# Performance work log

Measured on AMD Instinct MI355X. Metric: run time of the kernel, lower is better.

## Reference

```python
import jax, jax.numpy as jnp
import numpy as np

H = 16        # num_attention_heads
D = 1024      # hidden_size
HD = D // H   # head_dim = 64


def setup_inputs() -> dict:
    key = jax.random.key(0)
    ks = jax.random.split(key, 5)
    B, T = 16, 1024
    s_in = 1.0 / np.sqrt(D)
    return {
        "hidden_states": jax.random.normal(ks[0], (B, T, D), dtype=jnp.float32),
        "w_qkv": jax.random.normal(ks[1], (D, 3 * D), dtype=jnp.float32) * s_in,
        "b_qkv": jnp.zeros((3 * D,), dtype=jnp.float32),
        "w_out": jax.random.normal(ks[2], (D, D), dtype=jnp.float32) * s_in,
        "b_out": jnp.zeros((D,), dtype=jnp.float32),
    }


def reference(hidden_states, w_qkv, b_qkv, w_out, b_out):
    B, T, C = hidden_states.shape
    qkv = hidden_states @ w_qkv + b_qkv                      # [B,T,3C]
    q, k, v = jnp.split(qkv, 3, axis=-1)
    # [B,T,C] -> [B,H,T,HD]
    q = q.reshape(B, T, H, HD).transpose(0, 2, 1, 3)
    k = k.reshape(B, T, H, HD).transpose(0, 2, 1, 3)
    v = v.reshape(B, T, H, HD).transpose(0, 2, 1, 3)
    scale = 1.0 / np.sqrt(HD)
    logits = jnp.einsum("bhqd,bhkd->bhqk", q, k) * scale     # [B,H,T,T]
    attn = jax.nn.softmax(logits, axis=-1)
    out = jnp.einsum("bhqk,bhkd->bhqd", attn, v)             # [B,H,T,HD]
    out = out.transpose(0, 2, 1, 3).reshape(B, T, C)
    return out @ w_out + b_out
```

## Files before the change

kernel.cpp:

```cpp
#include <hip/hip_runtime.h>
#include <cstdint>
#include <cstddef>

typedef _Float16 h8 __attribute__((ext_vector_type(8)));
typedef _Float16 h4 __attribute__((ext_vector_type(4)));
typedef float f4 __attribute__((ext_vector_type(4)));
typedef float fx16 __attribute__((ext_vector_type(16)));

#define MFMA(a, b, c) __builtin_amdgcn_mfma_f32_16x16x32_f16((a), (b), (c), 0, 0, 0)
#define MFMA32(a, b, c) __builtin_amdgcn_mfma_f32_32x32x16_f16((a), (b), (c), 0, 0, 0)

__device__ __forceinline__ void gl_lds16(const void* g, void* l) {
  __builtin_amdgcn_global_load_lds((const __attribute__((address_space(1))) void*)g,
                                   (__attribute__((address_space(3))) void*)l, 16, 0, 0);
}

__global__ void k_cvt_hs(const float* __restrict__ in, _Float16* __restrict__ out, int n8) {
  int i = blockIdx.x * blockDim.x + threadIdx.x;
  if (i >= n8) return;
  size_t idx = (size_t)i * 8;
  float4 a = *(const float4*)(in + idx);
  float4 b = *(const float4*)(in + idx + 4);
  h8 o;
  o[0] = (_Float16)a.x; o[1] = (_Float16)a.y; o[2] = (_Float16)a.z; o[3] = (_Float16)a.w;
  o[4] = (_Float16)b.x; o[5] = (_Float16)b.y; o[6] = (_Float16)b.z; o[7] = (_Float16)b.w;
  *(h8*)(out + idx) = o;
}

__global__ void k_transcvt(const float* __restrict__ in, _Float16* __restrict__ out, int N, int K) {
  __shared__ float tile[64 * 65];
  int tn = blockIdx.x * 64, tk = blockIdx.y * 64;
  for (int i = 0; i < 4; ++i) {
    int cid = i * 256 + threadIdx.x;
    int r = cid >> 4, c4 = cid & 15;
    float4 v = *(const float4*)(in + (size_t)(tk + r) * N + tn + c4 * 4);
    tile[r * 65 + c4 * 4 + 0] = v.x; tile[r * 65 + c4 * 4 + 1] = v.y;
    tile[r * 65 + c4 * 4 + 2] = v.z; tile[r * 65 + c4 * 4 + 3] = v.w;
  }
  __syncthreads();
  for (int i = 0; i < 2; ++i) {
    int cid = i * 256 + threadIdx.x;
    int n = cid >> 3, kc = cid & 7;
    h8 o;
    for (int j = 0; j < 8; ++j) o[j] = (_Float16)tile[(kc * 8 + j) * 65 + n];
    *(h8*)(out + (size_t)(tn + n) * K + tk + kc * 8) = o;
  }
}

__global__ __launch_bounds__(256) void k_gemm_qkv(
    const _Float16* __restrict__ A, const _Float16* __restrict__ BT,
    const float* __restrict__ bias,
    _Float16* __restrict__ Q, _Float16* __restrict__ Kq, _Float16* __restrict__ Vt) {
  __shared__ char smem[32768];
  _Float16* sA = (_Float16*)smem;
  _Float16* sB = (_Float16*)(smem + 16384);
  const int K = 1024;
  int tid = threadIdx.x, wave = tid >> 6, lane = tid & 63;
  int l31 = lane & 31, l32h = lane >> 5;
  int tm = blockIdx.y * 128, tn = blockIdx.x * 128;
  int wm = (wave & 1) * 64, wn = (wave >> 1) * 64;
  fx16 acc[2][2] = {};
  for (int kt = 0; kt < K; kt += 64) {
    __syncthreads();
    for (int i = 0; i < 4; ++i) {
      int cid = i * 256 + tid;
      int r = cid >> 3, cs = cid & 7, cg = cs ^ (r & 7);
      gl_lds16(A + (size_t)(tm + r) * K + kt + cg * 8, (char*)sA + cid * 16);
      gl_lds16(BT + (size_t)(tn + r) * K + kt + cg * 8, (char*)sB + cid * 16);
    }
    __syncthreads();
    for (int k0 = 0; k0 < 64; k0 += 16) {
      h8 af[2], bf[2];
      int ch = (k0 >> 3) + l32h;
      for (int mi = 0; mi < 2; ++mi) {
        int r = wm + mi * 32 + l31;
        af[mi] = *(const h8*)((const char*)sA + ((r * 8 + (ch ^ (r & 7))) * 16));
      }
      for (int ni = 0; ni < 2; ++ni) {
        int r = wn + ni * 32 + l31;
        bf[ni] = *(const h8*)((const char*)sB + ((r * 8 + (ch ^ (r & 7))) * 16));
      }
      for (int mi = 0; mi < 2; ++mi)
        for (int ni = 0; ni < 2; ++ni)
          acc[mi][ni] = MFMA32(af[mi], bf[ni], acc[mi][ni]);
    }
  }
  if (blockIdx.x < 16) {
    for (int ni = 0; ni < 2; ++ni) {
      int n = tn + wn + ni * 32 + l31;
      float bv = bias[n];
      int which = n >> 10, h = (n >> 6) & 15, d = n & 63;
      _Float16* dst = which == 0 ? Q : Kq;
      for (int mi = 0; mi < 2; ++mi) {
        for (int g = 0; g < 4; ++g) {
          for (int rr = 0; rr < 4; ++rr) {
            int m = tm + wm + mi * 32 + rr + 8 * g + 4 * l32h;
            int b = m >> 10, t = m & 1023;
            dst[(((size_t)b * 16 + h) * 1024 + t) * 64 + d] =
                (_Float16)(acc[mi][ni][g * 4 + rr] + bv);
          }
        }
      }
    }
  } else {
    _Float16* L = (_Float16*)smem;
    int b = tm >> 10, tbase = tm & 1023;
    for (int pass = 0; pass < 2; ++pass) {
      __syncthreads();
      if ((wave & 1) == pass) {
        for (int mi = 0; mi < 2; ++mi) {
          for (int ni = 0; ni < 2; ++ni) {
            int n_local = wn + ni * 32 + l31;
            float bv = bias[tn + n_local];
            for (int g = 0; g < 4; ++g) {
              h4 pk;
              for (int rr = 0; rr < 4; ++rr)
                pk[rr] = (_Float16)(acc[mi][ni][g * 4 + rr] + bv);
              *(h4*)(L + n_local * 68 + mi * 32 + 8 * g + 4 * l32h) = pk;
            }
          }
        }
      }
      __syncthreads();
      for (int it = 0; it < 2; ++it) {
        int n_local = it * 64 + (tid >> 2);
        int h = (tn - 2048 + n_local) >> 6;
        int d = n_local & 63;
        size_t row = (((size_t)b * 16 + h) * 64 + d) * 1024 + tbase + pass * 64;
        for (int j = 0; j < 2; ++j) {
          int th = (tid & 3) * 8 + j * 32;
          *(h8*)(Vt + row + th) = *(const h8*)(L + n_local * 68 + th);
        }
      }
    }
  }
}

__global__ __launch_bounds__(256, 2) void k_attn(
    const _Float16* __restrict__ Q, const _Float16* __restrict__ Kk,
    const _Float16* __restrict__ Vt, _Float16* __restrict__ O) {
  __shared__ char smem[32768 + 8192 + 8192];
  _Float16* sQ = (_Float16*)smem;
  _Float16* sP = (_Float16*)smem;
  _Float16* sK = (_Float16*)(smem + 32768);
  _Float16* sV = (_Float16*)(smem + 32768 + 8192);
  const float SCL = 0.125f * 1.44269504088896340736f;
  int tid = threadIdx.x, wave = tid >> 6, lane = tid & 63;
  int l15 = lane & 15, l4 = lane >> 4;
  int bh = blockIdx.y;
  int qt = blockIdx.x * 256;
  const _Float16* Qb = Q + (size_t)bh * 65536;
  const _Float16* Kb = Kk + (size_t)bh * 65536;
  const _Float16* Vb = Vt + (size_t)bh * 65536;

  for (int i = 0; i < 8; ++i) {
    int cid = i * 256 + tid;
    int r = cid >> 3, cs = cid & 7, cg = cs ^ (r & 7);
    gl_lds16(Qb + (size_t)(qt + r) * 64 + cg * 8, (char*)sQ + cid * 16);
  }
  __syncthreads();
  h8 qf[4][2];
  for (int nt = 0; nt < 4; ++nt) {
    int r = wave * 64 + nt * 16 + l15;
    for (int kk = 0; kk < 2; ++kk) {
      int ch = kk * 4 + l4;
      qf[nt][kk] = *(const h8*)((const char*)sQ + ((r * 8 + (ch ^ (r & 7))) * 16));
    }
  }
  _Float16 scl_h = (_Float16)SCL;
  for (int nt = 0; nt < 4; ++nt)
    for (int kk = 0; kk < 2; ++kk)
      for (int j = 0; j < 8; ++j) qf[nt][kk][j] *= scl_h;

  int cid0 = tid, cid1 = tid + 256;
  int r0 = cid0 >> 3, c0 = (cid0 & 7) ^ (r0 & 7);
  int r1 = cid1 >> 3, c1 = (cid1 & 7) ^ (r1 & 7);
  const _Float16* kp0 = Kb + (size_t)r0 * 64 + c0 * 8;
  const _Float16* kp1 = Kb + (size_t)r1 * 64 + c1 * 8;
  const _Float16* vp0 = Vb + (size_t)r0 * 1024 + c0 * 8;
  const _Float16* vp1 = Vb + (size_t)r1 * 1024 + c1 * 8;
  char* dK0 = (char*)sK + cid0 * 16; char* dK1 = (char*)sK + cid1 * 16;
  char* dV0 = (char*)sV + cid0 * 16; char* dV1 = (char*)sV + cid1 * 16;

  f4 oacc[4][4] = {};
  f4 lacc[4] = {};
  h8 ones;
  for (int j = 0; j < 8; ++j) ones[j] = (_Float16)1.0f;
  _Float16* pw = sP + wave * 64 * 40;

  for (int kt = 0; kt < 1024; kt += 64) {
    __syncthreads();
    gl_lds16(kp0, dK0); gl_lds16(kp1, dK1);
    gl_lds16(vp0, dV0); gl_lds16(vp1, dV1);
    kp0 += 4096; kp1 += 4096; vp0 += 64; vp1 += 64;
    __syncthreads();
    for (int mh = 0; mh < 2; ++mh) {
      f4 sacc[2][4] = {};
      for (int kk = 0; kk < 2; ++kk) {
        h8 kf[2];
        int ch = kk * 4 + l4;
        for (int mt = 0; mt < 2; ++mt) {
          int r = mh * 32 + mt * 16 + l15;
          kf[mt] = *(const h8*)((const char*)sK + ((r * 8 + (ch ^ (r & 7))) * 16));
        }
        for (int mt = 0; mt < 2; ++mt)
          for (int nt = 0; nt < 4; ++nt)
            sacc[mt][nt] = MFMA(kf[mt], qf[nt][kk], sacc[mt][nt]);
      }
      for (int mt = 0; mt < 2; ++mt) {
        for (int nt = 0; nt < 4; ++nt) {
          float p0 = exp2f(sacc[mt][nt][0]);
          float p1 = exp2f(sacc[mt][nt][1]);
          float p2 = exp2f(sacc[mt][nt][2]);
          float p3 = exp2f(sacc[mt][nt][3]);
          h4 pk;
          pk[0] = (_Float16)p0; pk[1] = (_Float16)p1;
          pk[2] = (_Float16)p2; pk[3] = (_Float16)p3;
          *(h4*)(pw + (nt * 16 + l15) * 40 + mt * 16 + l4 * 4) = pk;
        }
      }
      h8 pf[4], vf[4];
      for (int mi = 0; mi < 4; ++mi)
        pf[mi] = *(const h8*)(pw + (mi * 16 + l15) * 40 + l4 * 8);
      int ch = mh * 4 + l4;
      for (int nd = 0; nd < 4; ++nd) {
        int r = nd * 16 + l15;
        vf[nd] = *(const h8*)((const char*)sV + ((r * 8 + (ch ^ (r & 7))) * 16));
      }
      for (int mi = 0; mi < 4; ++mi) {
        for (int nd = 0; nd < 4; ++nd)
          oacc[mi][nd] = MFMA(pf[mi], vf[nd], oacc[mi][nd]);
        lacc[mi] = MFMA(pf[mi], ones, lacc[mi]);
      }
    }
  }
  int b = bh >> 4, h = bh & 15;
  for (int mi = 0; mi < 4; ++mi) {
    for (int r = 0; r < 4; ++r) {
      float inv = 1.f / lacc[mi][r];
      int t = qt + wave * 64 + mi * 16 + l4 * 4 + r;
      for (int nd = 0; nd < 4; ++nd)
        O[(size_t)(b * 1024 + t) * 1024 + h * 64 + nd * 16 + l15] =
            (_Float16)(oacc[mi][nd][r] * inv);
    }
  }
}

__global__ __launch_bounds__(256) void k_gemm_out(
    const _Float16* __restrict__ A, const _Float16* __restrict__ BT,
    const float* __restrict__ bias, float* __restrict__ C) {
  __shared__ _Float16 sA[128 * 64];
  __shared__ _Float16 sB[128 * 64];
  const int K = 1024;
  int tid = threadIdx.x, wave = tid >> 6, lane = tid & 63;
  int l31 = lane & 31, l32h = lane >> 5;
  int tm = blockIdx.y * 128, tn = blockIdx.x * 128;
  int wm = (wave & 1) * 64, wn = (wave >> 1) * 64;
  fx16 acc[2][2] = {};
  for (int kt = 0; kt < K; kt += 64) {
    __syncthreads();
    for (int i = 0; i < 4; ++i) {
      int cid = i * 256 + tid;
      int r = cid >> 3, cs = cid & 7, cg = cs ^ (r & 7);
      gl_lds16(A + (size_t)(tm + r) * K + kt + cg * 8, (char*)sA + cid * 16);
      gl_lds16(BT + (size_t)(tn + r) * K + kt + cg * 8, (char*)sB + cid * 16);
    }
    __syncthreads();
    for (int k0 = 0; k0 < 64; k0 += 16) {
      h8 af[2], bf[2];
      int ch = (k0 >> 3) + l32h;
      for (int mi = 0; mi < 2; ++mi) {
        int r = wm + mi * 32 + l31;
        af[mi] = *(const h8*)((const char*)sA + ((r * 8 + (ch ^ (r & 7))) * 16));
      }
      for (int ni = 0; ni < 2; ++ni) {
        int r = wn + ni * 32 + l31;
        bf[ni] = *(const h8*)((const char*)sB + ((r * 8 + (ch ^ (r & 7))) * 16));
      }
      for (int mi = 0; mi < 2; ++mi)
        for (int ni = 0; ni < 2; ++ni)
          acc[mi][ni] = MFMA32(af[mi], bf[ni], acc[mi][ni]);
    }
  }
  for (int ni = 0; ni < 2; ++ni) {
    int n = tn + wn + ni * 32 + l31;
    float bv = bias[n];
    for (int mi = 0; mi < 2; ++mi) {
      for (int g = 0; g < 4; ++g) {
        for (int rr = 0; rr < 4; ++rr) {
          int m = tm + wm + mi * 32 + rr + 8 * g + 4 * l32h;
          C[(size_t)m * 1024 + n] = acc[mi][ni][g * 4 + rr] + bv;
        }
      }
    }
  }
}

extern "C" void kernel_launch(void* const* d_in, const int* in_sizes, int n_in,
                              void* d_out, int out_size, void* d_ws, size_t ws_size,
                              hipStream_t stream) {
  const float* hs    = (const float*)d_in[0];
  const float* w_qkv = (const float*)d_in[1];
  const float* b_qkv = (const float*)d_in[2];
  const float* w_out = (const float*)d_in[3];
  const float* b_out = (const float*)d_in[4];
  float* out = (float*)d_out;
  char* ws = (char*)d_ws;

  _Float16* hs_h  = (_Float16*)(ws);
  _Float16* wqkvT = (_Float16*)(ws + 33554432);
  _Float16* woutT = (_Float16*)(ws + 39845888);
  _Float16* q_ws  = (_Float16*)(ws + 41943040);
  _Float16* k_ws  = (_Float16*)(ws + 75497472);
  _Float16* vt_ws = (_Float16*)(ws + 109051904);

  k_cvt_hs<<<8192, 256, 0, stream>>>(hs, hs_h, 2097152);
  k_transcvt<<<dim3(48, 16), 256, 0, stream>>>(w_qkv, wqkvT, 3072, 1024);
  k_transcvt<<<dim3(16, 16), 256, 0, stream>>>(w_out, woutT, 1024, 1024);
  k_gemm_qkv<<<dim3(24, 128), 256, 0, stream>>>(hs_h, wqkvT, b_qkv, q_ws, k_ws, vt_ws);
  _Float16* attn_h = hs_h;
  k_attn<<<dim3(4, 256), 256, 0, stream>>>(q_ws, k_ws, vt_ws, attn_h);
  k_gemm_out<<<dim3(8, 128), 256, 0, stream>>>(attn_h, woutT, b_out, out);
}
```

Measured before the change: 425.4 us.

## Rewrite projection GEMMs as 256x256 double-buffered pipelined tiles with 512 threads

After: 388.3 us. -8.7%, faster.

```diff
diff --git a/kernel.cpp b/kernel.cpp
--- a/kernel.cpp
+++ b/kernel.cpp
@@ -5,14 +5,22 @@
 typedef _Float16 h8 __attribute__((ext_vector_type(8)));
 typedef _Float16 h4 __attribute__((ext_vector_type(4)));
 typedef float f4 __attribute__((ext_vector_type(4)));
-typedef float fx16 __attribute__((ext_vector_type(16)));
 
 #define MFMA(a, b, c) __builtin_amdgcn_mfma_f32_16x16x32_f16((a), (b), (c), 0, 0, 0)
-#define MFMA32(a, b, c) __builtin_amdgcn_mfma_f32_32x32x16_f16((a), (b), (c), 0, 0, 0)
 
 __device__ __forceinline__ void gl_lds16(const void* g, void* l) {
   __builtin_amdgcn_global_load_lds((const __attribute__((address_space(1))) void*)g,
                                    (__attribute__((address_space(3))) void*)l, 16, 0, 0);
+}
+
+__device__ __forceinline__ h8 lds_frag(const char* base, int r, int ch) {
+  return *(const h8*)(base + ((r * 8 + (ch ^ (r & 7))) * 16));
+}
+
+__device__ __forceinline__ void BAR() {
+  asm volatile("" ::: "memory");
+  __builtin_amdgcn_s_barrier();
+  asm volatile("" ::: "memory");
 }
 
 __global__ void k_cvt_hs(const float* __restrict__ in, _Float16* __restrict__ out, int n8) {
@@ -47,90 +55,184 @@
   }
 }
 
-__global__ __launch_bounds__(256) void k_gemm_qkv(
+__device__ __forceinline__ void gemm256_mainloop(
+    const _Float16* __restrict__ A, const _Float16* __restrict__ BT,
+    char* smem, int tm, int tn, f4 (&acc)[8][4]) {
+  int tid = threadIdx.x, lane = tid & 63, wave = tid >> 6;
+  int l15 = lane & 15, l4 = lane >> 4;
+  int wm = (wave >> 2) * 128, wn = (wave & 3) * 64;
+  const _Float16* Ab = A + (size_t)tm * 1024;
+  const _Float16* Bb = BT + (size_t)tn * 1024;
+  int r0 = tid >> 3, cg = (tid & 7) ^ (r0 & 7);
+  char* cA = smem;           char* nA = smem + 32768;
+  char* cB = smem + 65536;   char* nB = smem + 98304;
+
+  auto stA = [&](int kt, int h, char* dst) {
+    const _Float16* s = Ab + (size_t)(h * 128 + r0) * 1024 + kt + cg * 8;
+    gl_lds16(s, dst + h * 16384 + tid * 16);
+    gl_lds16(s + 64 * 1024, dst + h * 16384 + 8192 + tid * 16);
+  };
+  auto stB = [&](int kt, int h, char* dst) {
+    const _Float16* s = Bb + (size_t)(h * 128 + r0) * 1024 + kt + cg * 8;
+    gl_lds16(s, dst + h * 16384 + tid * 16);
+    gl_lds16(s + 64 * 1024, dst + h * 16384 + 8192 + tid * 16);
+  };
+
+  stA(0, 0, cA); stA(0, 1, cA);
+  stB(0, 0, cB); stB(0, 1, cB);
+  stB(64, 0, nB); stB(64, 1, nB);
+  asm volatile("s_waitcnt vmcnt(4)" ::: "memory");
+  BAR();
+
+  h8 af[4][2], bf[4][2];
+  for (int u = 0; u < 16; ++u) {
+    int kt1 = (u + 1) << 6, kt2 = (u + 2) << 6;
+#pragma unroll
+    for (int mi = 0; mi < 4; ++mi) {
+      int r = wm + mi * 16 + l15;
+      af[mi][0] = lds_frag(cA, r, l4);
+      af[mi][1] = lds_frag(cA, r, 4 + l4);
+    }
+#pragma unroll
+    for (int nj = 0; nj < 2; ++nj) {
+      int r = wn + nj * 16 + l15;
+      bf[nj][0] = lds_frag(cB, r, l4);
+      bf[nj][1] = lds_frag(cB, r, 4 + l4);
+    }
+    if (u < 15) stA(kt1, 0, nA);
+    asm volatile("s_waitcnt lgkmcnt(8)" ::: "memory");
+    BAR();
+    asm volatile("s_waitcnt lgkmcnt(0)" ::: "memory");
+    __builtin_amdgcn_s_setprio(1);
+#pragma unroll
+    for (int kk = 0; kk < 2; ++kk)
+#pragma unroll
+      for (int mi = 0; mi < 4; ++mi)
+#pragma unroll
+        for (int nj = 0; nj < 2; ++nj)
+          acc[mi][nj] = MFMA(af[mi][kk], bf[nj][kk], acc[mi][nj]);
+    __builtin_amdgcn_s_setprio(0);
+    BAR();
+#pragma unroll
+    for (int nj = 2; nj < 4; ++nj) {
+      int r = wn + nj * 16 + l15;
+      bf[nj][0] = lds_frag(cB, r, l4);
+      bf[nj][1] = lds_frag(cB, r, 4 + l4);
+    }
+    if (u < 15) stA(kt1, 1, nA);
+    BAR();
+    asm volatile("s_waitcnt lgkmcnt(0)" ::: "memory");
+    __builtin_amdgcn_s_setprio(1);
+#pragma unroll
+    for (int kk = 0; kk < 2; ++kk)
+#pragma unroll
+      for (int mi = 0; mi < 4; ++mi)
+#pragma unroll
+        for (int nj = 2; nj < 4; ++nj)
+          acc[mi][nj] = MFMA(af[mi][kk], bf[nj][kk], acc[mi][nj]);
+    __builtin_amdgcn_s_setprio(0);
+    BAR();
+#pragma unroll
+    for (int mi = 0; mi < 4; ++mi) {
+      int r = wm + 64 + mi * 16 + l15;
+      af[mi][0] = lds_frag(cA, r, l4);
+      af[mi][1] = lds_frag(cA, r, 4 + l4);
+    }
+    if (u < 14) stB(kt2, 0, cB);
+    BAR();
+    asm volatile("s_waitcnt lgkmcnt(0)" ::: "memory");
+    __builtin_amdgcn_s_setprio(1);
+#pragma unroll
+    for (int kk = 0; kk < 2; ++kk)
+#pragma unroll
+      for (int mi = 0; mi < 4; ++mi)
+#pragma unroll
+        for (int nj = 2; nj < 4; ++nj)
+          acc[4 + mi][nj] = MFMA(af[mi][kk], bf[nj][kk], acc[4 + mi][nj]);
+    __builtin_amdgcn_s_setprio(0);
+    BAR();
+    if (u < 14) stB(kt2, 1, cB);
+    if (u < 14) asm volatile("s_waitcnt vmcnt(4)" ::: "memory");
+    else        asm volatile("s_waitcnt vmcnt(0)" ::: "memory");
+    BAR();
+    __builtin_amdgcn_s_setprio(1);
+#pragma unroll
+    for (int kk = 0; kk < 2; ++kk)
+#pragma unroll
+      for (int mi = 0; mi < 4; ++mi)
+#pragma unroll
+        for (int nj = 0; nj < 2; ++nj)
+          acc[4 + mi][nj] = MFMA(af[mi][kk], bf[nj][kk], acc[4 + mi][nj]);
+    __builtin_amdgcn_s_setprio(0);
+    BAR();
+    char* t = cA; cA = nA; nA = t;
+    t = cB; cB = nB; nB = t;
+  }
+}
+
+__global__ __launch_bounds__(512) void k_gemm_qkv(
     const _Float16* __restrict__ A, const _Float16* __restrict__ BT,
     const float* __restrict__ bias,
     _Float16* __restrict__ Q, _Float16* __restrict__ Kq, _Float16* __restrict__ Vt) {
-  __shared__ char smem[32768];
-  _Float16* sA = (_Float16*)smem;
-  _Float16* sB = (_Float16*)(smem + 16384);
-  const int K = 1024;
-  int tid = threadIdx.x, wave = tid >> 6, lane = tid & 63;
-  int l31 = lane & 31, l32h = lane >> 5;
-  int tm = blockIdx.y * 128, tn = blockIdx.x * 128;
-  int wm = (wave & 1) * 64, wn = (wave >> 1) * 64;
-  fx16 acc[2][2] = {};
-  for (int kt = 0; kt < K; kt += 64) {
-    __syncthreads();
-    for (int i = 0; i < 4; ++i) {
-      int cid = i * 256 + tid;
-      int r = cid >> 3, cs = cid & 7, cg = cs ^ (r & 7);
-      gl_lds16(A + (size_t)(tm + r) * K + kt + cg * 8, (char*)sA + cid * 16);
-      gl_lds16(BT + (size_t)(tn + r) * K + kt + cg * 8, (char*)sB + cid * 16);
-    }
-    __syncthreads();
-    for (int k0 = 0; k0 < 64; k0 += 16) {
-      h8 af[2], bf[2];
-      int ch = (k0 >> 3) + l32h;
-      for (int mi = 0; mi < 2; ++mi) {
-        int r = wm + mi * 32 + l31;
-        af[mi] = *(const h8*)((const char*)sA + ((r * 8 + (ch ^ (r & 7))) * 16));
-      }
-      for (int ni = 0; ni < 2; ++ni) {
-        int r = wn + ni * 32 + l31;
-        bf[ni] = *(const h8*)((const char*)sB + ((r * 8 + (ch ^ (r & 7))) * 16));
-      }
-      for (int mi = 0; mi < 2; ++mi)
-        for (int ni = 0; ni < 2; ++ni)
-          acc[mi][ni] = MFMA32(af[mi], bf[ni], acc[mi][ni]);
-    }
-  }
-  if (blockIdx.x < 16) {
-    for (int ni = 0; ni < 2; ++ni) {
-      int n = tn + wn + ni * 32 + l31;
+  __shared__ char smem[131072];
+  int id = blockIdx.x;
+  int swz = (id & 7) * 96 + (id >> 3);
+  int by = swz / 12, bx = swz - by * 12;
+  int tm = by * 256, tn = bx * 256;
+  f4 acc[8][4] = {};
+  gemm256_mainloop(A, BT, smem, tm, tn, acc);
+
+  int tid = threadIdx.x, lane = tid & 63, wave = tid >> 6;
+  int l15 = lane & 15, l4 = lane >> 4;
+  int wm = (wave >> 2) * 128, wn = (wave & 3) * 64;
+  if (tn < 2048) {
+    _Float16* dst = (tn >= 1024) ? Kq : Q;
+#pragma unroll
+    for (int nj = 0; nj < 4; ++nj) {
+      int n = tn + wn + nj * 16 + l15;
       float bv = bias[n];
-      int which = n >> 10, h = (n >> 6) & 15, d = n & 63;
-      _Float16* dst = which == 0 ? Q : Kq;
-      for (int mi = 0; mi < 2; ++mi) {
-        for (int g = 0; g < 4; ++g) {
-          for (int rr = 0; rr < 4; ++rr) {
-            int m = tm + wm + mi * 32 + rr + 8 * g + 4 * l32h;
-            int b = m >> 10, t = m & 1023;
-            dst[(((size_t)b * 16 + h) * 1024 + t) * 64 + d] =
-                (_Float16)(acc[mi][ni][g * 4 + rr] + bv);
+      int h = (n >> 6) & 15, d = n & 63;
+#pragma unroll
+      for (int mig = 0; mig < 8; ++mig) {
+#pragma unroll
+        for (int r = 0; r < 4; ++r) {
+          int m = tm + wm + mig * 16 + l4 * 4 + r;
+          int b = m >> 10, t = m & 1023;
+          dst[(((size_t)b * 16 + h) * 1024 + t) * 64 + d] =
+              (_Float16)(acc[mig][nj][r] + bv);
+        }
+      }
+    }
+  } else {
+    _Float16* L = (_Float16*)smem;
+    int b = tm >> 10, tb = tm & 1023;
+#pragma unroll
+    for (int p = 0; p < 2; ++p) {
+      __syncthreads();
+      if (((wave >> 1) & 1) == p) {
+        int nloc = (wave & 1) * 64;
+#pragma unroll
+        for (int nj = 0; nj < 4; ++nj) {
+          int nl = nloc + nj * 16 + l15;
+          float bv = bias[tn + p * 128 + nl];
+#pragma unroll
+          for (int mig = 0; mig < 8; ++mig) {
+            h4 pk;
+#pragma unroll
+            for (int r = 0; r < 4; ++r) pk[r] = (_Float16)(acc[mig][nj][r] + bv);
+            *(h4*)(L + nl * 264 + wm + mig * 16 + l4 * 4) = pk;
           }
         }
       }
-    }
-  } else {
-    _Float16* L = (_Float16*)smem;
-    int b = tm >> 10, tbase = tm & 1023;
-    for (int pass = 0; pass < 2; ++pass) {
       __syncthreads();
-      if ((wave & 1) == pass) {
-        for (int mi = 0; mi < 2; ++mi) {
-          for (int ni = 0; ni < 2; ++ni) {
-            int n_local = wn + ni * 32 + l31;
-            float bv = bias[tn + n_local];
-            for (int g = 0; g < 4; ++g) {
-              h4 pk;
-              for (int rr = 0; rr < 4; ++rr)
-                pk[rr] = (_Float16)(acc[mi][ni][g * 4 + rr] + bv);
-              *(h4*)(L + n_local * 68 + mi * 32 + 8 * g + 4 * l32h) = pk;
-            }
-          }
-        }
-      }
-      __syncthreads();
-      for (int it = 0; it < 2; ++it) {
-        int n_local = it * 64 + (tid >> 2);
-        int h = (tn - 2048 + n_local) >> 6;
-        int d = n_local & 63;
-        size_t row = (((size_t)b * 16 + h) * 64 + d) * 1024 + tbase + pass * 64;
-        for (int j = 0; j < 2; ++j) {
-          int th = (tid & 3) * 8 + j * 32;
-          *(h8*)(Vt + row + th) = *(const h8*)(L + n_local * 68 + th);
-        }
+#pragma unroll
+      for (int i = 0; i < 8; ++i) {
+        int cid = i * 512 + tid;
+        int nl = cid >> 5, tc = cid & 31;
+        int ng = tn + p * 128 + nl;
+        int h = (ng >> 6) & 15, d = ng & 63;
+        *(h8*)(Vt + (((size_t)b * 16 + h) * 64 + d) * 1024 + tb + tc * 8) =
+            *(const h8*)(L + nl * 264 + tc * 8);
       }
     }
   }
@@ -246,51 +348,30 @@
   }
 }
 
-__global__ __launch_bounds__(256) void k_gemm_out(
+__global__ __launch_bounds__(512) void k_gemm_out(
     const _Float16* __restrict__ A, const _Float16* __restrict__ BT,
     const float* __restrict__ bias, float* __restrict__ C) {
-  __shared__ _Float16 sA[128 * 64];
-  __shared__ _Float16 sB[128 * 64];
-  const int K = 1024;
-  int tid = threadIdx.x, wave = tid >> 6, lane = tid & 63;
-  int l31 = lane & 31, l32h = lane >> 5;
-  int tm = blockIdx.y * 128, tn = blockIdx.x * 128;
-  int wm = (wave & 1) * 64, wn = (wave >> 1) * 64;
-  fx16 acc[2][2] = {};
-  for (int kt = 0; kt < K; kt += 64) {
-    __syncthreads();
-    for (int i = 0; i < 4; ++i) {
-      int cid = i * 256 + tid;
-      int r = cid >> 3, cs = cid & 7, cg = cs ^ (r & 7);
-      gl_lds16(A + (size_t)(tm + r) * K + kt + cg * 8, (char*)sA + cid * 16);
-      gl_lds16(BT + (size_t)(tn + r) * K + kt + cg * 8, (char*)sB + cid * 16);
-    }
-    __syncthreads();
-    for (int k0 = 0; k0 < 64; k0 += 16) {
-      h8 af[2], bf[2];
-      int ch = (k0 >> 3) + l32h;
-      for (int mi = 0; mi < 2; ++mi) {
-        int r = wm + mi * 32 + l31;
-        af[mi] = *(const h8*)((const char*)sA + ((r * 8 + (ch ^ (r & 7))) * 16));
-      }
-      for (int ni = 0; ni < 2; ++ni) {
-        int r = wn + ni * 32 + l31;
-        bf[ni] = *(const h8*)((const char*)sB + ((r * 8 + (ch ^ (r & 7))) * 16));
-      }
-      for (int mi = 0; mi < 2; ++mi)
-        for (int ni = 0; ni < 2; ++ni)
-          acc[mi][ni] = MFMA32(af[mi], bf[ni], acc[mi][ni]);
-    }
-  }
-  for (int ni = 0; ni < 2; ++ni) {
-    int n = tn + wn + ni * 32 + l31;
+  __shared__ char smem[131072];
+  int id = blockIdx.x;
+  int swz = (id & 7) * 32 + (id >> 3);
+  int by = swz >> 2, bx = swz & 3;
+  int tm = by * 256, tn = bx * 256;
+  f4 acc[8][4] = {};
+  gemm256_mainloop(A, BT, smem, tm, tn, acc);
+
+  int tid = threadIdx.x, lane = tid & 63, wave = tid >> 6;
+  int l15 = lane & 15, l4 = lane >> 4;
+  int wm = (wave >> 2) * 128, wn = (wave & 3) * 64;
+#pragma unroll
+  for (int nj = 0; nj < 4; ++nj) {
+    int n = tn + wn + nj * 16 + l15;
     float bv = bias[n];
-    for (int mi = 0; mi < 2; ++mi) {
-      for (int g = 0; g < 4; ++g) {
-        for (int rr = 0; rr < 4; ++rr) {
-          int m = tm + wm + mi * 32 + rr + 8 * g + 4 * l32h;
-          C[(size_t)m * 1024 + n] = acc[mi][ni][g * 4 + rr] + bv;
-        }
+#pragma unroll
+    for (int mig = 0; mig < 8; ++mig) {
+#pragma unroll
+      for (int r = 0; r < 4; ++r) {
+        int m = tm + wm + mig * 16 + l4 * 4 + r;
+        C[(size_t)m * 1024 + n] = acc[mig][nj][r] + bv;
       }
     }
   }
@@ -317,8 +398,8 @@
   k_cvt_hs<<<8192, 256, 0, stream>>>(hs, hs_h, 2097152);
   k_transcvt<<<dim3(48, 16), 256, 0, stream>>>(w_qkv, wqkvT, 3072, 1024);
   k_transcvt<<<dim3(16, 16), 256, 0, stream>>>(w_out, woutT, 1024, 1024);
-  k_gemm_qkv<<<dim3(24, 128), 256, 0, stream>>>(hs_h, wqkvT, b_qkv, q_ws, k_ws, vt_ws);
+  k_gemm_qkv<<<768, 512, 0, stream>>>(hs_h, wqkvT, b_qkv, q_ws, k_ws, vt_ws);
   _Float16* attn_h = hs_h;
   k_attn<<<dim3(4, 256), 256, 0, stream>>>(q_ws, k_ws, vt_ws, attn_h);
-  k_gemm_out<<<dim3(8, 128), 256, 0, stream>>>(attn_h, woutT, b_out, out);
-}
+  k_gemm_out<<<256, 512, 0, stream>>>(attn_h, woutT, b_out, out);
+}
```
